# Kernel tuning notes

Hardware: AMD Instinct MI355X
Metric: run time of the kernel (lower is better)

Reference implementation:

```python
import jax, jax.numpy as jnp
import numpy as np

N_NODES = 10000
N_EDGES = 60000
D = 128          # latent_size
L = 15           # num_layers
EPS = 1e-5       # LayerNorm eps (torch default)


def _layernorm(h, g, b):
    mu = jnp.mean(h, axis=-1, keepdims=True)
    var = jnp.mean(jnp.square(h - mu), axis=-1, keepdims=True)
    return (h - mu) * jax.lax.rsqrt(var + EPS) * g + b


def _mlp(h, w1, b1, g1, bt1, w2, b2, g2, bt2):
    # Linear -> LayerNorm -> GELU(exact) -> [Dropout: identity in eval] -> Linear -> LayerNorm
    h = _layernorm(h @ w1 + b1, g1, bt1)
    h = jax.nn.gelu(h, approximate=False)
    return _layernorm(h @ w2 + b2, g2, bt2)


def setup_inputs() -> dict:
    key = jax.random.key(0)
    ks = jax.random.split(key, 20)
    x = jax.random.normal(ks[0], (N_NODES, D), dtype=jnp.float32)
    edge_index = jax.random.randint(ks[1], (2, N_EDGES), 0, N_NODES, dtype=jnp.int32)
    edge_attr = jax.random.normal(ks[2], (N_EDGES, D), dtype=jnp.float32)
    s = 0.02
    # Edge MLP params: Linear(3D->2D), LN(2D), Linear(2D->D), LN(D), stacked over L layers
    ew1 = jax.random.normal(ks[3], (L, 3 * D, 2 * D), dtype=jnp.float32) * s
    eb1 = jnp.zeros((L, 2 * D), dtype=jnp.float32)
    eg1 = jnp.ones((L, 2 * D), dtype=jnp.float32)
    ebt1 = jnp.zeros((L, 2 * D), dtype=jnp.float32)
    ew2 = jax.random.normal(ks[4], (L, 2 * D, D), dtype=jnp.float32) * s
    eb2 = jnp.zeros((L, D), dtype=jnp.float32)
    eg2 = jnp.ones((L, D), dtype=jnp.float32)
    ebt2 = jnp.zeros((L, D), dtype=jnp.float32)
    # Node MLP params: Linear(2D->2D), LN(2D), Linear(2D->D), LN(D)
    nw1 = jax.random.normal(ks[5], (L, 2 * D, 2 * D), dtype=jnp.float32) * s
    nb1 = jnp.zeros((L, 2 * D), dtype=jnp.float32)
    ng1 = jnp.ones((L, 2 * D), dtype=jnp.float32)
    nbt1 = jnp.zeros((L, 2 * D), dtype=jnp.float32)
    nw2 = jax.random.normal(ks[6], (L, 2 * D, D), dtype=jnp.float32) * s
    nb2 = jnp.zeros((L, D), dtype=jnp.float32)
    ng2 = jnp.ones((L, D), dtype=jnp.float32)
    nbt2 = jnp.zeros((L, D), dtype=jnp.float32)
    return dict(x=x, edge_index=edge_index, edge_attr=edge_attr,
                ew1=ew1, eb1=eb1, eg1=eg1, ebt1=ebt1, ew2=ew2, eb2=eb2, eg2=eg2, ebt2=ebt2,
                nw1=nw1, nb1=nb1, ng1=ng1, nbt1=nbt1, nw2=nw2, nb2=nb2, ng2=ng2, nbt2=nbt2)


def reference(x, edge_index, edge_attr,
              ew1, eb1, eg1, ebt1, ew2, eb2, eg2, ebt2,
              nw1, nb1, ng1, nbt1, nw2, nb2, ng2, nbt2):
    row, col = edge_index[0], edge_index[1]
    # neighbor counts (per destination node), clamped to >= 1; constant across layers
    count = jax.ops.segment_sum(jnp.ones((edge_index.shape[1],), dtype=x.dtype), col,
                                num_segments=x.shape[0])
    count = jnp.maximum(count, 1.0)[:, None]  # [N,1]
    for i in range(L):
        edge_input = jnp.concatenate([x[row], x[col], edge_attr], axis=1)  # [E, 3D]
        edge_attr = edge_attr + _mlp(edge_input, ew1[i], eb1[i], eg1[i], ebt1[i],
                                     ew2[i], eb2[i], eg2[i], ebt2[i])
        agg = jax.ops.segment_sum(edge_attr, col, num_segments=x.shape[0]) / count  # [N, D]
        node_input = jnp.concatenate([x, agg], axis=1)  # [N, 2D]
        x = x + _mlp(node_input, nw1[i], nb1[i], ng1[i], nbt1[i],
                     nw2[i], nb2[i], ng2[i], nbt2[i])
    return x, edge_attr
```

## Files before the change

kernel.cpp:

```cpp
#include <hip/hip_runtime.h>
#include <hip/hip_bf16.h>
#include <math.h>

#define NN 10000
#define NE 60000
#define DD 128
#define NL 15
#define LN_EPS 1e-5f

typedef __attribute__((ext_vector_type(8))) short short8;
typedef __attribute__((ext_vector_type(4))) float floatx4;

__device__ __forceinline__ unsigned short f2bf(float f) {
    unsigned u = __float_as_uint(f);
    u += 0x7fff + ((u >> 16) & 1);
    return (unsigned short)(u >> 16);
}
__device__ __forceinline__ unsigned bc2(float a, float b) {
    __hip_bfloat162 t = __float22bfloat162_rn(make_float2(a, b));
    return *(unsigned*)&t;
}
__device__ __forceinline__ float gelu_fast(float y) {
    float u = y * y;
    float s2 = y * fmaf(u, 0.07135481283f, 1.59576912161f);
    return y * __builtin_amdgcn_rcpf(1.0f + __expf(-s2));
}

__device__ __forceinline__ void pack_one(const float* __restrict__ W, unsigned short* __restrict__ P,
                                         int u, int Kk, int Nk, bool perm) {
    int per_layer = Kk * Nk;
    int i = u / per_layer;
    int v0 = u - i * per_layer;
    int S = Kk >> 5;
    int t = v0 / (S * 512);
    int rem = v0 - t * (S * 512);
    int s = rem >> 9;
    int v = rem & 511;
    int l = v >> 3, j = v & 7;
    int kv = (s << 5) + ((l >> 4) << 3) + j;
    int k = perm ? (((kv & 15) << 4) | (kv >> 4)) : kv;
    int n = (t << 4) + (l & 15);
    P[u] = f2bf(W[((size_t)i * Kk + k) * Nk + n]);
}

#define N_EW1 (NL * 384 * 256)
#define N_EW2 (NL * 256 * 128)
#define N_NW1 (NL * 256 * 256)
#define N_NW2 (NL * 256 * 128)

__global__ void pack_all(const float* __restrict__ ew1, const float* __restrict__ ew2,
                         const float* __restrict__ nw1, const float* __restrict__ nw2,
                         unsigned short* __restrict__ P) {
    int tid = blockIdx.x * blockDim.x + threadIdx.x;
    if (tid < N_EW1) { pack_one(ew1, P, tid, 384, 256, false); return; }
    tid -= N_EW1;
    if (tid < N_EW2) { pack_one(ew2, P + N_EW1, tid, 256, 128, true); return; }
    tid -= N_EW2;
    if (tid < N_NW1) { pack_one(nw1, P + N_EW1 + N_EW2, tid, 256, 256, false); return; }
    tid -= N_NW1;
    if (tid < N_NW2) { pack_one(nw2, P + N_EW1 + N_EW2 + N_NW1, tid, 256, 128, true); return; }
}

__global__ void hist_kernel(const int* __restrict__ ecol, int* __restrict__ cnt) {
    int e = blockIdx.x * blockDim.x + threadIdx.x;
    if (e < NE) atomicAdd(&cnt[ecol[e]], 1);
}

__global__ void scan_kernel(const int* __restrict__ cnt, int* __restrict__ starts,
                            int* __restrict__ cursor, float* __restrict__ cinv) {
    __shared__ int part[256];
    int t = threadIdx.x;
    const int chunk = (NN + 255) / 256;
    int lo = t * chunk;
    int hi = lo + chunk; if (hi > NN) hi = NN;
    int s = 0;
    for (int n = lo; n < hi; ++n) s += cnt[n];
    part[t] = s;
    __syncthreads();
    for (int off = 1; off < 256; off <<= 1) {
        int v = (t >= off) ? part[t - off] : 0;
        __syncthreads();
        part[t] += v;
        __syncthreads();
    }
    int base = part[t] - s;
    for (int n = lo; n < hi; ++n) {
        int c = cnt[n];
        starts[n] = base; cursor[n] = base;
        cinv[n] = 1.0f / (float)(c > 0 ? c : 1);
        base += c;
    }
}

__global__ void fill_kernel(const int* __restrict__ ecol, int* __restrict__ cursor,
                            int* __restrict__ eidx) {
    int e = blockIdx.x * blockDim.x + threadIdx.x;
    if (e < NE) {
        int slot = atomicAdd(&cursor[ecol[e]], 1);
        eidx[slot] = e;
    }
}

__global__ void init_shadow(const float* __restrict__ x, unsigned short* __restrict__ xb) {
    int t = blockIdx.x * blockDim.x + threadIdx.x;
    const int NX = NN * DD / 4;
    if (t < NX) {
        float4 v = *(const float4*)&x[(size_t)t * 4];
        uint2 p; p.x = bc2(v.x, v.y); p.y = bc2(v.z, v.w);
        *(uint2*)&xb[(size_t)t * 4] = p;
    }
}

template <int K1, int ROWS_TOTAL, int ROWS, bool EDGE>
__global__ __launch_bounds__(ROWS * 8, 4)
void mlp_mfma(const unsigned short* __restrict__ xb16,
              const int* __restrict__ erow, const int* __restrict__ ecol,
              const float* __restrict__ easrc,
              const int* __restrict__ starts, const int* __restrict__ cnt,
              const float* __restrict__ cinv, const int* __restrict__ eidx,
              float* __restrict__ target,
              unsigned short* __restrict__ shadow,
              const unsigned short* __restrict__ W1p, const unsigned short* __restrict__ W2p,
              const float* __restrict__ b1, const float* __restrict__ g1, const float* __restrict__ bt1,
              const float* __restrict__ b2, const float* __restrict__ g2, const float* __restrict__ bt2)
{
    constexpr int S1 = K1 / 32;
    __shared__ union {
        unsigned short a1[ROWS * K1];
        unsigned short h[ROWS * 256];
    } sm;
    __shared__ float red1[ROWS][8];
    __shared__ float red2[ROWS][8];

    const int tid  = threadIdx.x;
    const int lane = tid & 63;
    const int w    = tid >> 6;
    const int q    = lane >> 4;
    const int c15  = lane & 15;
    const int r0   = blockIdx.x * ROWS;

    const int qn = w & 3;
    const int pm = w >> 2;
    const int mp = w >> 2;
    const int np = w & 3;

    {
        const int r = tid >> 3;
        const int g = tid & 7;
        const int row_g = r0 + r;
        const bool ok = (ROWS_TOTAL % ROWS == 0) || (row_g < ROWS_TOTAL);
        const int rg = ok ? row_g : 0;
        if constexpr (EDGE) {
            const unsigned short* baseA = &xb16[(size_t)erow[rg] * DD];
            const unsigned short* baseB = &xb16[(size_t)ecol[rg] * DD];
            const float* baseC = &easrc[(size_t)rg * DD];
            #pragma unroll
            for (int it = 0; it < 6; ++it) {
                const int gg = g + 8 * it;
                const int p = gg << 3;
                uint4 v;
                if (p < 128) {
                    v = *(const uint4*)(baseA + p);
                } else if (p < 256) {
                    v = *(const uint4*)(baseB + (p - 128));
                } else {
                    float4 f0 = *(const float4*)(baseC + (p - 256));
                    float4 f1 = *(const float4*)(baseC + (p - 252));
                    v.x = bc2(f0.x, f0.y); v.y = bc2(f0.z, f0.w);
                    v.z = bc2(f1.x, f1.y); v.w = bc2(f1.z, f1.w);
                }
                *(uint4*)&sm.a1[r * K1 + ((gg ^ (r & 7)) << 3)] = v;
            }
        } else {
            const unsigned short* baseA = &xb16[(size_t)rg * DD];
            #pragma unroll
            for (int it = 0; it < 2; ++it) {
                const int gg = g + 8 * it;
                uint4 v = *(const uint4*)(baseA + (gg << 3));
                *(uint4*)&sm.a1[r * K1 + ((gg ^ (r & 7)) << 3)] = v;
            }
            const int st = starts[rg];
            const int de = cnt[rg];
            const float ci = cinv[rg];
            float4 sa0 = {0.f,0.f,0.f,0.f}, sa1 = sa0, sb0 = sa0, sb1 = sa0;
            for (int i = 0; i < de; ++i) {
                const int e = eidx[st + i];
                const float* er = &easrc[(size_t)e * DD + (g << 3)];
                float4 a0 = *(const float4*)(er);
                float4 a1 = *(const float4*)(er + 4);
                float4 b0 = *(const float4*)(er + 64);
                float4 b1 = *(const float4*)(er + 68);
                sa0.x += a0.x; sa0.y += a0.y; sa0.z += a0.z; sa0.w += a0.w;
                sa1.x += a1.x; sa1.y += a1.y; sa1.z += a1.z; sa1.w += a1.w;
                sb0.x += b0.x; sb0.y += b0.y; sb0.z += b0.z; sb0.w += b0.w;
                sb1.x += b1.x; sb1.y += b1.y; sb1.z += b1.z; sb1.w += b1.w;
            }
            uint4 v;
            v.x = bc2(sa0.x * ci, sa0.y * ci); v.y = bc2(sa0.z * ci, sa0.w * ci);
            v.z = bc2(sa1.x * ci, sa1.y * ci); v.w = bc2(sa1.z * ci, sa1.w * ci);
            const int gg2 = g + 16;
            *(uint4*)&sm.a1[r * K1 + ((gg2 ^ (r & 7)) << 3)] = v;
            v.x = bc2(sb0.x * ci, sb0.y * ci); v.y = bc2(sb0.z * ci, sb0.w * ci);
            v.z = bc2(sb1.x * ci, sb1.y * ci); v.w = bc2(sb1.z * ci, sb1.w * ci);
            const int gg3 = g + 24;
            *(uint4*)&sm.a1[r * K1 + ((gg3 ^ (r & 7)) << 3)] = v;
        }
    }
    __syncthreads();

    float b2c[2], g2c[2], t2c[2];
    #pragma unroll
    for (int jn = 0; jn < 2; ++jn) {
        int col = (((np << 1) + jn) << 4) + c15;
        b2c[jn] = b2[col]; g2c[jn] = g2[col]; t2c[jn] = bt2[col];
    }

    floatx4 acc[2][4];
    #pragma unroll
    for (int mt = 0; mt < 2; ++mt)
        #pragma unroll
        for (int ntl = 0; ntl < 4; ++ntl)
            acc[mt][ntl] = (floatx4){0.f, 0.f, 0.f, 0.f};

    __builtin_amdgcn_s_setprio(1);
    #pragma unroll
    for (int s = 0; s < S1; ++s) {
        short8 af[2];
        #pragma unroll
        for (int mt = 0; mt < 2; ++mt) {
            int row  = (((pm << 1) + mt) << 4) + c15;
            int kgrp = ((s << 2) + q) ^ (row & 7);
            af[mt] = *(const short8*)&sm.a1[row * K1 + (kgrp << 3)];
        }
        #pragma unroll
        for (int ntl = 0; ntl < 4; ++ntl) {
            const short8 bf = *(const short8*)&W1p[((((((qn << 2) + ntl) * S1) + s) << 6) + lane) << 3];
            #pragma unroll
            for (int mt = 0; mt < 2; ++mt)
                acc[mt][ntl] = __builtin_amdgcn_mfma_f32_16x16x32_bf16(af[mt], bf, acc[mt][ntl], 0, 0, 0);
        }
    }
    __builtin_amdgcn_s_setprio(0);

    float b1c[4], g1c[4], t1c[4];
    #pragma unroll
    for (int ntl = 0; ntl < 4; ++ntl) {
        int col = (((qn << 2) + ntl) << 4) + c15;
        b1c[ntl] = b1[col]; g1c[ntl] = g1[col]; t1c[ntl] = bt1[col];
    }
    #pragma unroll
    for (int mt = 0; mt < 2; ++mt)
        #pragma unroll
        for (int r = 0; r < 4; ++r) {
            float p = 0.f, sq = 0.f;
            #pragma unroll
            for (int ntl = 0; ntl < 4; ++ntl) {
                float v = acc[mt][ntl][r] + b1c[ntl];
                acc[mt][ntl][r] = v;
                p += v; sq += v * v;
            }
            p += __shfl_xor(p, 1);  sq += __shfl_xor(sq, 1);
            p += __shfl_xor(p, 2);  sq += __shfl_xor(sq, 2);
            p += __shfl_xor(p, 4);  sq += __shfl_xor(sq, 4);
            p += __shfl_xor(p, 8);  sq += __shfl_xor(sq, 8);
            if (c15 == 0) {
                int row = (((pm << 1) + mt) << 4) + (q << 2) + r;
                red1[row][(qn << 1) + 0] = p;
                red1[row][(qn << 1) + 1] = sq;
            }
        }
    __syncthreads();

    #pragma unroll
    for (int mt = 0; mt < 2; ++mt)
        #pragma unroll
        for (int r = 0; r < 4; ++r) {
            int row = (((pm << 1) + mt) << 4) + (q << 2) + r;
            const float4 p0 = *(const float4*)&red1[row][0];
            const float4 p1 = *(const float4*)&red1[row][4];
            float p  = p0.x + p0.z + p1.x + p1.z;
            float sq = p0.y + p0.w + p1.y + p1.w;
            float mu = p * (1.0f / 256.0f);
            float rs = rsqrtf(sq * (1.0f / 256.0f) - mu * mu + LN_EPS);
            float y0 = gelu_fast((acc[mt][0][r] - mu) * rs * g1c[0] + t1c[0]);
            float y1 = gelu_fast((acc[mt][1][r] - mu) * rs * g1c[1] + t1c[1]);
            float y2 = gelu_fast((acc[mt][2][r] - mu) * rs * g1c[2] + t1c[2]);
            float y3 = gelu_fast((acc[mt][3][r] - mu) * rs * g1c[3] + t1c[3]);
            uint2 hp;
            hp.x = bc2(y0, y1);
            hp.y = bc2(y2, y3);
            int gg = (c15 << 1) + (qn >> 1);
            int addr = row * 256 + (((gg ^ (row & 7)) << 3) | ((qn & 1) << 2));
            *(uint2*)&sm.h[addr] = hp;
        }
    __syncthreads();

    floatx4 acc2[2][2];
    #pragma unroll
    for (int jm = 0; jm < 2; ++jm)
        #pragma unroll
        for (int jn = 0; jn < 2; ++jn)
            acc2[jm][jn] = (floatx4){0.f, 0.f, 0.f, 0.f};

    __builtin_amdgcn_s_setprio(1);
    #pragma unroll
    for (int s = 0; s < 8; ++s) {
        short8 a2[2];
        #pragma unroll
        for (int jm = 0; jm < 2; ++jm) {
            int mrow = (((mp << 1) + jm) << 4) + c15;
            int kgrp = ((s << 2) + q) ^ (mrow & 7);
            a2[jm] = *(const short8*)&sm.h[mrow * 256 + (kgrp << 3)];
        }
        #pragma unroll
        for (int jn = 0; jn < 2; ++jn) {
            int nt = (np << 1) + jn;
            const short8 b = *(const short8*)&W2p[((((nt << 3) + s) << 6) + lane) << 3];
            #pragma unroll
            for (int jm = 0; jm < 2; ++jm)
                acc2[jm][jn] = __builtin_amdgcn_mfma_f32_16x16x32_bf16(a2[jm], b, acc2[jm][jn], 0, 0, 0);
        }
    }
    __builtin_amdgcn_s_setprio(0);

    float tpre[2][4][2];
    #pragma unroll
    for (int jm = 0; jm < 2; ++jm)
        #pragma unroll
        for (int r = 0; r < 4; ++r) {
            int row = (((mp << 1) + jm) << 4) + (q << 2) + r;
            int rowg = r0 + row;
            const bool okk = (ROWS_TOTAL % ROWS == 0) || (rowg < ROWS_TOTAL);
            const int rgs = okk ? rowg : 0;
            #pragma unroll
            for (int jn = 0; jn < 2; ++jn) {
                int col = (((np << 1) + jn) << 4) + c15;
                tpre[jm][r][jn] = target[(size_t)rgs * DD + col];
            }
        }

    #pragma unroll
    for (int jm = 0; jm < 2; ++jm)
        #pragma unroll
        for (int r = 0; r < 4; ++r) {
            float p = 0.f, sq = 0.f;
            #pragma unroll
            for (int jn = 0; jn < 2; ++jn) {
                float v = acc2[jm][jn][r] + b2c[jn];
                acc2[jm][jn][r] = v;
                p += v; sq += v * v;
            }
            p += __shfl_xor(p, 1);  sq += __shfl_xor(sq, 1);
            p += __shfl_xor(p, 2);  sq += __shfl_xor(sq, 2);
            p += __shfl_xor(p, 4);  sq += __shfl_xor(sq, 4);
            p += __shfl_xor(p, 8);  sq += __shfl_xor(sq, 8);
            if (c15 == 0) {
                int row = (((mp << 1) + jm) << 4) + (q << 2) + r;
                red2[row][(np << 1) + 0] = p;
                red2[row][(np << 1) + 1] = sq;
            }
        }
    __syncthreads();

    #pragma unroll
    for (int jm = 0; jm < 2; ++jm)
        #pragma unroll
        for (int r = 0; r < 4; ++r) {
            int row = (((mp << 1) + jm) << 4) + (q << 2) + r;
            const float4 pp0 = *(const float4*)&red2[row][0];
            const float4 pp1 = *(const float4*)&red2[row][4];
            float p  = pp0.x + pp0.z + pp1.x + pp1.z;
            float sq = pp0.y + pp0.w + pp1.y + pp1.w;
            float mu = p * (1.0f / 128.0f);
            float rs = rsqrtf(sq * (1.0f / 128.0f) - mu * mu + LN_EPS);
            int rowg = r0 + row;
            if (ROWS_TOTAL % ROWS == 0 || rowg < ROWS_TOTAL) {
                #pragma unroll
                for (int jn = 0; jn < 2; ++jn) {
                    int col = (((np << 1) + jn) << 4) + c15;
                    float o = (acc2[jm][jn][r] - mu) * rs * g2c[jn] + t2c[jn];
                    float t = tpre[jm][r][jn] + o;
                    target[(size_t)rowg * DD + col] = t;
                    if constexpr (!EDGE)
                        shadow[(size_t)rowg * DD + col] = f2bf(t);
                }
            }
        }
}

extern "C" void kernel_launch(void* const* d_in, const int* in_sizes, int n_in,
                              void* d_out, int out_size, void* d_ws, size_t ws_size,
                              hipStream_t stream) {
    const float* x_in  = (const float*)d_in[0];
    const int*   ei    = (const int*)  d_in[1];
    const float* ea_in = (const float*)d_in[2];
    const float* ew1 = (const float*)d_in[3];
    const float* eb1 = (const float*)d_in[4];
    const float* eg1 = (const float*)d_in[5];
    const float* ebt1= (const float*)d_in[6];
    const float* ew2 = (const float*)d_in[7];
    const float* eb2 = (const float*)d_in[8];
    const float* eg2 = (const float*)d_in[9];
    const float* ebt2= (const float*)d_in[10];
    const float* nw1 = (const float*)d_in[11];
    const float* nb1 = (const float*)d_in[12];
    const float* ng1 = (const float*)d_in[13];
    const float* nbt1= (const float*)d_in[14];
    const float* nw2 = (const float*)d_in[15];
    const float* nb2 = (const float*)d_in[16];
    const float* ng2 = (const float*)d_in[17];
    const float* nbt2= (const float*)d_in[18];

    const int* erow = ei;
    const int* ecol = ei + NE;

    float* xbuf  = (float*)d_out;
    float* eabuf = (float*)d_out + NN * DD;

    unsigned short* ew1p  = (unsigned short*)d_ws;
    unsigned short* ew2p  = ew1p + N_EW1;
    unsigned short* nw1p  = ew2p + N_EW2;
    unsigned short* nw2p  = nw1p + N_NW1;
    unsigned short* xb16  = nw2p + N_NW2;
    int*   cnt    = (int*)(xb16 + (size_t)NN * DD);
    int*   starts = cnt + NN;
    int*   cursor = starts + NN;
    int*   eidx   = cursor + NN;
    float* cinv   = (float*)(eidx + NE);

    hipMemcpyAsync(xbuf,  x_in,  (size_t)NN * DD * sizeof(float), hipMemcpyDeviceToDevice, stream);
    hipMemcpyAsync(eabuf, ea_in, (size_t)NE * DD * sizeof(float), hipMemcpyDeviceToDevice, stream);

    hipMemsetAsync(cnt, 0, NN * sizeof(int), stream);
    hist_kernel<<<(NE + 255) / 256, 256, 0, stream>>>(ecol, cnt);
    scan_kernel<<<1, 256, 0, stream>>>(cnt, starts, cursor, cinv);
    fill_kernel<<<(NE + 255) / 256, 256, 0, stream>>>(ecol, cursor, eidx);

    init_shadow<<<(NN * DD / 4 + 255) / 256, 256, 0, stream>>>(x_in, xb16);

    {
        int ntot = N_EW1 + N_EW2 + N_NW1 + N_NW2;
        pack_all<<<(ntot + 255) / 256, 256, 0, stream>>>(ew1, ew2, nw1, nw2, ew1p);
    }

    for (int i = 0; i < NL; ++i) {
        mlp_mfma<384, NE, 32, true><<<NE / 32, 256, 0, stream>>>(
            xb16, erow, ecol, eabuf, nullptr, nullptr, nullptr, nullptr,
            eabuf, nullptr,
            ew1p + (size_t)i * 384 * 256, ew2p + (size_t)i * 256 * 128,
            eb1 + (size_t)i * 256, eg1 + (size_t)i * 256, ebt1 + (size_t)i * 256,
            eb2 + (size_t)i * 128, eg2 + (size_t)i * 128, ebt2 + (size_t)i * 128);
        mlp_mfma<256, NN, 32, false><<<(NN + 31) / 32, 256, 0, stream>>>(
            xb16, nullptr, nullptr, eabuf, starts, cnt, cinv, eidx,
            xbuf, xb16,
            nw1p + (size_t)i * 256 * 256, nw2p + (size_t)i * 256 * 128,
            nb1 + (size_t)i * 256, ng1 + (size_t)i * 256, nbt1 + (size_t)i * 256,
            nb2 + (size_t)i * 128, ng2 + (size_t)i * 128, nbt2 + (size_t)i * 128);
    }
}
```

Measured before the change: 1.178 ms.

## Store edge features as bf16 shadow and skip fp32 edge writes until last layer

Edge attributes are kept only as a bf16 shadow buffer across layers. The edge kernel reads that buffer directly, takes the residual term from the bf16 values already staged in shared memory, and writes fp32 output only on the final layer. The node aggregation also gathers bf16 edge rows, which halves that gather's traffic. This cuts edge-feature memory traffic in both kernels but stores the residual stream in bf16, so rounding error builds up over 15 layers and accuracy may suffer.

```diff
diff --git a/kernel.cpp b/kernel.cpp
--- a/kernel.cpp
+++ b/kernel.cpp
@@ -20,6 +20,8 @@
     __hip_bfloat162 t = __float22bfloat162_rn(make_float2(a, b));
     return *(unsigned*)&t;
 }
+__device__ __forceinline__ float bfl(unsigned w) { return __uint_as_float(w << 16); }
+__device__ __forceinline__ float bfh(unsigned w) { return __uint_as_float(w & 0xffff0000u); }
 __device__ __forceinline__ float gelu_fast(float y) {
     float u = y * y;
     float s2 = y * fmaf(u, 0.07135481283f, 1.59576912161f);
@@ -101,13 +103,20 @@
     }
 }
 
-__global__ void init_shadow(const float* __restrict__ x, unsigned short* __restrict__ xb) {
+__global__ void init_shadow(const float* __restrict__ x, const float* __restrict__ ea,
+                            unsigned short* __restrict__ xb, unsigned short* __restrict__ eb) {
     int t = blockIdx.x * blockDim.x + threadIdx.x;
     const int NX = NN * DD / 4;
+    const int NEA = NE * DD / 4;
     if (t < NX) {
         float4 v = *(const float4*)&x[(size_t)t * 4];
         uint2 p; p.x = bc2(v.x, v.y); p.y = bc2(v.z, v.w);
         *(uint2*)&xb[(size_t)t * 4] = p;
+    } else if (t < NX + NEA) {
+        size_t u = (size_t)(t - NX);
+        float4 v = *(const float4*)&ea[u * 4];
+        uint2 p; p.x = bc2(v.x, v.y); p.y = bc2(v.z, v.w);
+        *(uint2*)&eb[u * 4] = p;
     }
 }
 
@@ -115,7 +124,7 @@
 __global__ __launch_bounds__(ROWS * 8, 4)
 void mlp_mfma(const unsigned short* __restrict__ xb16,
               const int* __restrict__ erow, const int* __restrict__ ecol,
-              const float* __restrict__ easrc,
+              const unsigned short* __restrict__ eas16,
               const int* __restrict__ starts, const int* __restrict__ cnt,
               const float* __restrict__ cinv, const int* __restrict__ eidx,
               float* __restrict__ target,
@@ -153,22 +162,15 @@
         if constexpr (EDGE) {
             const unsigned short* baseA = &xb16[(size_t)erow[rg] * DD];
             const unsigned short* baseB = &xb16[(size_t)ecol[rg] * DD];
-            const float* baseC = &easrc[(size_t)rg * DD];
+            const unsigned short* baseC = &eas16[(size_t)rg * DD];
             #pragma unroll
             for (int it = 0; it < 6; ++it) {
                 const int gg = g + 8 * it;
                 const int p = gg << 3;
-                uint4 v;
-                if (p < 128) {
-                    v = *(const uint4*)(baseA + p);
-                } else if (p < 256) {
-                    v = *(const uint4*)(baseB + (p - 128));
-                } else {
-                    float4 f0 = *(const float4*)(baseC + (p - 256));
-                    float4 f1 = *(const float4*)(baseC + (p - 252));
-                    v.x = bc2(f0.x, f0.y); v.y = bc2(f0.z, f0.w);
-                    v.z = bc2(f1.x, f1.y); v.w = bc2(f1.z, f1.w);
-                }
+                const unsigned short* src = (p < 128) ? (baseA + p)
+                                          : (p < 256) ? (baseB + (p - 128))
+                                                      : (baseC + (p - 256));
+                uint4 v = *(const uint4*)src;
                 *(uint4*)&sm.a1[r * K1 + ((gg ^ (r & 7)) << 3)] = v;
             }
         } else {
@@ -185,15 +187,13 @@
             float4 sa0 = {0.f,0.f,0.f,0.f}, sa1 = sa0, sb0 = sa0, sb1 = sa0;
             for (int i = 0; i < de; ++i) {
                 const int e = eidx[st + i];
-                const float* er = &easrc[(size_t)e * DD + (g << 3)];
-                float4 a0 = *(const float4*)(er);
-                float4 a1 = *(const float4*)(er + 4);
-                float4 b0 = *(const float4*)(er + 64);
-                float4 b1 = *(const float4*)(er + 68);
-                sa0.x += a0.x; sa0.y += a0.y; sa0.z += a0.z; sa0.w += a0.w;
-                sa1.x += a1.x; sa1.y += a1.y; sa1.z += a1.z; sa1.w += a1.w;
-                sb0.x += b0.x; sb0.y += b0.y; sb0.z += b0.z; sb0.w += b0.w;
-                sb1.x += b1.x; sb1.y += b1.y; sb1.z += b1.z; sb1.w += b1.w;
+                const unsigned short* er = &eas16[(size_t)e * DD + (g << 3)];
+                uint4 a = *(const uint4*)er;
+                uint4 b = *(const uint4*)(er + 64);
+                sa0.x += bfl(a.x); sa0.y += bfh(a.x); sa0.z += bfl(a.y); sa0.w += bfh(a.y);
+                sa1.x += bfl(a.z); sa1.y += bfh(a.z); sa1.z += bfl(a.w); sa1.w += bfh(a.w);
+                sb0.x += bfl(b.x); sb0.y += bfh(b.x); sb0.z += bfl(b.y); sb0.w += bfh(b.y);
+                sb1.x += bfl(b.z); sb1.y += bfh(b.z); sb1.z += bfl(b.w); sb1.w += bfh(b.w);
             }
             uint4 v;
             v.x = bc2(sa0.x * ci, sa0.y * ci); v.y = bc2(sa0.z * ci, sa0.w * ci);
@@ -241,6 +241,23 @@
         }
     }
     __builtin_amdgcn_s_setprio(0);
+
+    float tpre[2][4][2];
+    if constexpr (EDGE) {
+        #pragma unroll
+        for (int jm = 0; jm < 2; ++jm)
+            #pragma unroll
+            for (int r = 0; r < 4; ++r) {
+                int row = (((mp << 1) + jm) << 4) + (q << 2) + r;
+                #pragma unroll
+                for (int jn = 0; jn < 2; ++jn) {
+                    int col = (((np << 1) + jn) << 4) + c15;
+                    int vc = 256 + col;
+                    int addr = row * K1 + ((((vc >> 3) ^ (row & 7)) << 3) | (vc & 7));
+                    tpre[jm][r][jn] = __uint_as_float((unsigned)sm.a1[addr] << 16);
+                }
+            }
+    }
 
     float b1c[4], g1c[4], t1c[4];
     #pragma unroll
@@ -323,21 +340,22 @@
     }
     __builtin_amdgcn_s_setprio(0);
 
-    float tpre[2][4][2];
-    #pragma unroll
-    for (int jm = 0; jm < 2; ++jm)
-        #pragma unroll
-        for (int r = 0; r < 4; ++r) {
-            int row = (((mp << 1) + jm) << 4) + (q << 2) + r;
-            int rowg = r0 + row;
-            const bool okk = (ROWS_TOTAL % ROWS == 0) || (rowg < ROWS_TOTAL);
-            const int rgs = okk ? rowg : 0;
-            #pragma unroll
-            for (int jn = 0; jn < 2; ++jn) {
-                int col = (((np << 1) + jn) << 4) + c15;
-                tpre[jm][r][jn] = target[(size_t)rgs * DD + col];
-            }
-        }
+    if constexpr (!EDGE) {
+        #pragma unroll
+        for (int jm = 0; jm < 2; ++jm)
+            #pragma unroll
+            for (int r = 0; r < 4; ++r) {
+                int row = (((mp << 1) + jm) << 4) + (q << 2) + r;
+                int rowg = r0 + row;
+                const bool okk = (ROWS_TOTAL % ROWS == 0) || (rowg < ROWS_TOTAL);
+                const int rgs = okk ? rowg : 0;
+                #pragma unroll
+                for (int jn = 0; jn < 2; ++jn) {
+                    int col = (((np << 1) + jn) << 4) + c15;
+                    tpre[jm][r][jn] = target[(size_t)rgs * DD + col];
+                }
+            }
+    }
 
     #pragma unroll
     for (int jm = 0; jm < 2; ++jm)
@@ -380,9 +398,12 @@
                     int col = (((np << 1) + jn) << 4) + c15;
                     float o = (acc2[jm][jn][r] - mu) * rs * g2c[jn] + t2c[jn];
                     float t = tpre[jm][r][jn] + o;
-                    target[(size_t)rowg * DD + col] = t;
-                    if constexpr (!EDGE)
-                        shadow[(size_t)rowg * DD + col] = f2bf(t);
+                    shadow[(size_t)rowg * DD + col] = f2bf(t);
+                    if constexpr (EDGE) {
+                        if (target) target[(size_t)rowg * DD + col] = t;
+                    } else {
+                        target[(size_t)rowg * DD + col] = t;
+                    }
                 }
             }
         }
@@ -422,21 +443,24 @@
     unsigned short* nw1p  = ew2p + N_EW2;
     unsigned short* nw2p  = nw1p + N_NW1;
     unsigned short* xb16  = nw2p + N_NW2;
-    int*   cnt    = (int*)(xb16 + (size_t)NN * DD);
+    unsigned short* eas16 = xb16 + (size_t)NN * DD;
+    int*   cnt    = (int*)(eas16 + (size_t)NE * DD);
     int*   starts = cnt + NN;
     int*   cursor = starts + NN;
     int*   eidx   = cursor + NN;
     float* cinv   = (float*)(eidx + NE);
 
-    hipMemcpyAsync(xbuf,  x_in,  (size_t)NN * DD * sizeof(float), hipMemcpyDeviceToDevice, stream);
-    hipMemcpyAsync(eabuf, ea_in, (size_t)NE * DD * sizeof(float), hipMemcpyDeviceToDevice, stream);
+    hipMemcpyAsync(xbuf, x_in, (size_t)NN * DD * sizeof(float), hipMemcpyDeviceToDevice, stream);
 
     hipMemsetAsync(cnt, 0, NN * sizeof(int), stream);
     hist_kernel<<<(NE + 255) / 256, 256, 0, stream>>>(ecol, cnt);
     scan_kernel<<<1, 256, 0, stream>>>(cnt, starts, cursor, cinv);
     fill_kernel<<<(NE + 255) / 256, 256, 0, stream>>>(ecol, cursor, eidx);
 
-    init_shadow<<<(NN * DD / 4 + 255) / 256, 256, 0, stream>>>(x_in, xb16);
+    {
+        int ntot = (NN * DD + NE * DD) / 4;
+        init_shadow<<<(ntot + 255) / 256, 256, 0, stream>>>(x_in, ea_in, xb16, eas16);
+    }
 
     {
         int ntot = N_EW1 + N_EW2 + N_NW1 + N_NW2;
@@ -445,13 +469,13 @@
 
     for (int i = 0; i < NL; ++i) {
         mlp_mfma<384, NE, 32, true><<<NE / 32, 256, 0, stream>>>(
-            xb16, erow, ecol, eabuf, nullptr, nullptr, nullptr, nullptr,
-            eabuf, nullptr,
+            xb16, erow, ecol, eas16, nullptr, nullptr, nullptr, nullptr,
+            (i == NL - 1) ? eabuf : nullptr, eas16,
             ew1p + (size_t)i * 384 * 256, ew2p + (size_t)i * 256 * 128,
             eb1 + (size_t)i * 256, eg1 + (size_t)i * 256, ebt1 + (size_t)i * 256,
             eb2 + (size_t)i * 128, eg2 + (size_t)i * 128, ebt2 + (size_t)i * 128);
         mlp_mfma<256, NN, 32, false><<<(NN + 31) / 32, 256, 0, stream>>>(
-            xb16, nullptr, nullptr, eabuf, starts, cnt, cinv, eidx,
+            xb16, nullptr, nullptr, eas16, starts, cnt, cinv, eidx,
             xbuf, xb16,
             nw1p + (size_t)i * 256 * 256, nw2p + (size_t)i * 256 * 128,
             nb1 + (size_t)i * 256, ng1 + (size_t)i * 256, nbt1 + (size_t)i * 256,
```

New measurement: 1.137 ms. -3.5%, faster.
